# Optimization experiments

Measured on AMD Instinct MI355X. Metric: run time of the kernel, lower is better.

## Reference

```python
import jax, jax.numpy as jnp
import numpy as np

NUM_ROIS = 148
BSZ = 16
HID = 64
IN_CH = 128
OUT_CH = 2
N1, E1 = 131072, 2097152
N2, E2 = 2368, 37888
LRELU_SLOPE = 0.01
BN_EPS = 1e-5


def gcn_conv(x, src, dst, ew, W, b, n):
    """PyG GCNConv with edge weights and self-loops (weight 1): D^-1/2 (A+I) D^-1/2 X W + b."""
    h = x @ W  # (n, out)
    deg = jax.ops.segment_sum(ew, dst, num_segments=n) + 1.0  # self-loop weight 1
    dinv = jax.lax.rsqrt(deg)
    norm = dinv[src] * ew * dinv[dst]  # (E,)
    out = jax.ops.segment_sum(h[src] * norm[:, None], dst, num_segments=n)
    out = out + h * (dinv * dinv)[:, None]  # self-loop term: 1/deg
    return out + b


def roi_pool_mean(x, roi, batch, num_rois, bsz):
    """Segment mean keyed by (batch, roi); empty groups stay zero. Returns (bsz, num_rois*d)."""
    seg = batch * num_rois + roi
    nseg = bsz * num_rois
    sums = jax.ops.segment_sum(x, seg, num_segments=nseg)
    cnt = jax.ops.segment_sum(jnp.ones((x.shape[0],), x.dtype), seg, num_segments=nseg)
    pooled = sums / jnp.maximum(cnt, 1.0)[:, None]
    return pooled.reshape(bsz, -1)


def _params(key):
    ks = jax.random.split(key, 8)
    def lin(k, fi, fo):
        return jax.random.normal(k, (fi, fo), jnp.float32) / np.sqrt(fi)
    p = {}
    p["W1a"], p["b1a"] = lin(ks[0], IN_CH, HID), jnp.zeros((HID,), jnp.float32)
    p["W1b"], p["b1b"] = lin(ks[1], HID, HID), jnp.zeros((HID,), jnp.float32)
    p["W2a"], p["b2a"] = lin(ks[2], IN_CH, HID), jnp.zeros((HID,), jnp.float32)
    p["W2b"], p["b2b"] = lin(ks[3], HID, HID), jnp.zeros((HID,), jnp.float32)
    p["Wm1"], p["bm1"] = lin(ks[4], HID * NUM_ROIS, 1000), jnp.zeros((1000,), jnp.float32)
    p["gamma"], p["beta"] = jnp.ones((1000,), jnp.float32), jnp.zeros((1000,), jnp.float32)
    p["bn_mean"], p["bn_var"] = jnp.zeros((1000,), jnp.float32), jnp.ones((1000,), jnp.float32)
    p["Wm2"], p["bm2"] = lin(ks[5], 1000, OUT_CH), jnp.zeros((OUT_CH,), jnp.float32)
    return p


def setup_inputs() -> dict:
    key = jax.random.key(0)
    ks = jax.random.split(key, 12)
    inp = {
        "x1": jax.random.normal(ks[0], (N1, IN_CH), jnp.float32),
        "node_label": jax.random.randint(ks[1], (N1,), 0, NUM_ROIS, jnp.int32),
        "edge_index1": jax.random.randint(ks[2], (2, E1), 0, N1, jnp.int32),
        "edge_weight1": jax.random.uniform(ks[3], (E1,), jnp.float32),
        "batch1": jnp.sort(jax.random.randint(ks[4], (N1,), 0, BSZ, jnp.int32)),
        "x2": jax.random.normal(ks[5], (N2, IN_CH), jnp.float32),
        "roi_label": jax.random.randint(ks[6], (N2,), 0, NUM_ROIS, jnp.int32),
        "edge_index2": jax.random.randint(ks[7], (2, E2), 0, N2, jnp.int32),
        "edge_weight2": jax.random.uniform(ks[8], (E2,), jnp.float32),
        "batch2": jnp.sort(jax.random.randint(ks[9], (N2,), 0, BSZ, jnp.int32)),
    }
    inp.update(_params(ks[10]))
    return inp


def reference(x1, node_label, edge_index1, edge_weight1, batch1,
              x2, roi_label, edge_index2, edge_weight2, batch2,
              W1a, b1a, W1b, b1b, W2a, b2a, W2b, b2b,
              Wm1, bm1, gamma, beta, bn_mean, bn_var, Wm2, bm2):
    # ROI-graph branch (convs_roi[:-1], eval mode: dropout is identity)
    s2, d2 = edge_index2[0], edge_index2[1]
    h2 = jax.nn.relu(gcn_conv(x2, s2, d2, edge_weight2, W2a, b2a, N2))
    h2 = jax.nn.relu(gcn_conv(h2, s2, d2, edge_weight2, W2b, b2b, N2))
    embedding_roi = roi_pool_mean(h2, roi_label, batch2, NUM_ROIS, BSZ)  # (B, 148*HID)
    # fine-grained branch (convs[:-1])
    s1, d1 = edge_index1[0], edge_index1[1]
    h1 = jax.nn.relu(gcn_conv(x1, s1, d1, edge_weight1, W1a, b1a, N1))
    h1 = jax.nn.relu(gcn_conv(h1, s1, d1, edge_weight1, W1b, b1b, N1))
    embedding = roi_pool_mean(h1, node_label, batch1, NUM_ROIS, BSZ)
    # classifier on embedding + embedding_roi
    s = embedding + embedding_roi
    h = s @ Wm1 + bm1
    h = gamma * (h - bn_mean) * jax.lax.rsqrt(bn_var + BN_EPS) + beta  # BatchNorm1d (eval)
    h = jnp.where(h > 0, h, LRELU_SLOPE * h)  # LeakyReLU
    out = h @ Wm2 + bm2  # (B, OUT_CH)
    return out, embedding, embedding_roi, embedding + embedding_roi
```

## Files before the change

### kernel.cpp

```cpp
#include <hip/hip_runtime.h>
#include <hip/hip_fp16.h>

#define N1 131072
#define E1 2097152
#define N2 2368
#define E2 37888
#define NROIS 148
#define BSZ 16
#define HID 64
#define INCH 128
#define NSEG (BSZ*NROIS)
#define SDIM (NROIS*HID)
#define CLS 1000
#define OCH 2

#define KT1 74
#define KCC 128
#define CT1 4

#define NB1 512
#define BLK1 512
#define EPB (E1/BLK1)
#define NPB (N1/NB1)

#define CB1 ((N1+3)/4)
#define CB2 ((N2+3)/4)
#define PB  ((NSEG+3)/4)

#define T1 (N1/16)
#define T2 (N2/16)
#define GEMMB ((T1+T2)/4)

typedef _Float16 h8 __attribute__((ext_vector_type(8)));
typedef float f4 __attribute__((ext_vector_type(4)));

__device__ __forceinline__ unsigned packh2(float a, float b) {
    return (unsigned)__half_as_ushort(__float2half_rn(a)) |
           ((unsigned)__half_as_ushort(__float2half_rn(b)) << 16);
}

__device__ __forceinline__ void fma_lo(float& a, unsigned hb, float w) {
    asm("v_fma_mix_f32 %0, %1, %2, %0 op_sel:[0,0,0] op_sel_hi:[1,0,0]"
        : "+v"(a) : "v"(hb), "v"(w));
}
__device__ __forceinline__ void fma_hi(float& a, unsigned hb, float w) {
    asm("v_fma_mix_f32 %0, %1, %2, %0 op_sel:[1,0,0] op_sel_hi:[1,0,0]"
        : "+v"(a) : "v"(hb), "v"(w));
}


__global__ void k_hist_dst(int* __restrict__ cnt, const int* __restrict__ dst, int E) {
    int e = blockIdx.x * 256 + threadIdx.x;
    if (e < E) atomicAdd(&cnt[dst[e]], 1);
}

__global__ void k_hist_seg2(int* __restrict__ c1, const int* __restrict__ b1,
                            const int* __restrict__ l1, int n1_,
                            int* __restrict__ c2, const int* __restrict__ b2,
                            const int* __restrict__ l2, int n2_) {
    int i = blockIdx.x * 256 + threadIdx.x;
    if (i < n1_) { atomicAdd(&c1[b1[i] * NROIS + l1[i]], 1); return; }
    int j = i - n1_;
    if (j < n2_) atomicAdd(&c2[b2[j] * NROIS + l2[j]], 1);
}

__global__ void k_scan1(const int* __restrict__ in, int* __restrict__ out,
                        int* __restrict__ part, int n) {
    __shared__ int sh[256];
    int t = threadIdx.x;
    int i0 = blockIdx.x * 1024 + t * 4;
    int v0 = (i0     < n) ? in[i0]     : 0;
    int v1 = (i0 + 1 < n) ? in[i0 + 1] : 0;
    int v2 = (i0 + 2 < n) ? in[i0 + 2] : 0;
    int v3 = (i0 + 3 < n) ? in[i0 + 3] : 0;
    int tot = v0 + v1 + v2 + v3;
    sh[t] = tot; __syncthreads();
    for (int off = 1; off < 256; off <<= 1) {
        int x = 0; if (t >= off) x = sh[t - off];
        __syncthreads();
        if (t >= off) sh[t] += x;
        __syncthreads();
    }
    int excl = sh[t] - tot;
    if (t == 255) part[blockIdx.x] = sh[255];
    if (i0     < n) out[i0]     = excl;
    if (i0 + 1 < n) out[i0 + 1] = excl + v0;
    if (i0 + 2 < n) out[i0 + 2] = excl + v0 + v1;
    if (i0 + 3 < n) out[i0 + 3] = excl + v0 + v1 + v2;
}

__global__ void k_scan2(int* __restrict__ part, int cnt) {
    __shared__ int sh[256];
    int t = threadIdx.x;
    int v = (t < cnt) ? part[t] : 0;
    sh[t] = v; __syncthreads();
    for (int off = 1; off < 256; off <<= 1) {
        int x = 0; if (t >= off) x = sh[t - off];
        __syncthreads();
        if (t >= off) sh[t] += x;
        __syncthreads();
    }
    if (t < cnt) part[t] = sh[t] - v;
}

__global__ void k_scan3(int* __restrict__ out, const int* __restrict__ part, int n, int total) {
    int i = blockIdx.x * 256 + threadIdx.x;
    if (i < n) out[i] += part[i >> 10];
    if (i == 0) out[n] = total;
}

__global__ void k_scan_one(const int* __restrict__ in0, int* __restrict__ out0,
                           int* __restrict__ oo0, int n0,
                           const int* __restrict__ in1, int* __restrict__ out1,
                           int* __restrict__ oo1, int n1_) {
    __shared__ int sh[256];
    __shared__ int carry;
    const int* in; int* out; int* oo; int n;
    if (blockIdx.x == 0) { in = in0; out = out0; oo = oo0; n = n0; }
    else { if (!in1) return; in = in1; out = out1; oo = oo1; n = n1_; }
    int t = threadIdx.x;
    if (t == 0) carry = 0;
    __syncthreads();
    for (int base = 0; base < n; base += 256) {
        int i = base + t;
        int v = (i < n) ? in[i] : 0;
        sh[t] = v; __syncthreads();
        for (int off = 1; off < 256; off <<= 1) {
            int x = 0; if (t >= off) x = sh[t - off];
            __syncthreads();
            if (t >= off) sh[t] += x;
            __syncthreads();
        }
        if (i < n) {
            int e = carry + sh[t] - v;
            out[i] = e;
            if (oo) oo[i] = e;
        }
        __syncthreads();
        if (t == 255) carry += sh[255];
        __syncthreads();
    }
    if (t == 0) out[n] = carry;
}

__global__ void k_fill_edges(int2* __restrict__ edges, int* __restrict__ off,
                             const int* __restrict__ src, const int* __restrict__ dst,
                             const float* __restrict__ ew, int E) {
    int e = blockIdx.x * 256 + threadIdx.x;
    if (e >= E) return;
    int pos = atomicAdd(&off[dst[e]], 1);
    edges[pos] = make_int2(src[e], __float_as_int(ew[e]));
}

__global__ void k_fill_seg2(int* __restrict__ id1, int* __restrict__ o1,
                            const int* __restrict__ b1, const int* __restrict__ l1, int n1_,
                            int* __restrict__ id2, int* __restrict__ o2,
                            const int* __restrict__ b2, const int* __restrict__ l2, int n2_) {
    int i = blockIdx.x * 256 + threadIdx.x;
    if (i < n1_) {
        int pos = atomicAdd(&o1[b1[i] * NROIS + l1[i]], 1);
        id1[pos] = i << 7;
        return;
    }
    int j = i - n1_;
    if (j < n2_) {
        int pos = atomicAdd(&o2[b2[j] * NROIS + l2[j]], 1);
        id2[pos] = j << 7;
    }
}

__global__ void k_deg_dinv(float* __restrict__ dinv, const int* __restrict__ row,
                           const int2* __restrict__ edges, int n) {
    int d = blockIdx.x * 256 + threadIdx.x;
    if (d >= n) return;
    int a = row[d], b = row[d + 1];
    float s = 1.0f;
    for (int i = a; i < b; i++) s += __int_as_float(edges[i].y);
    dinv[d] = rsqrtf(s);
}

__global__ void k_scale(int2* __restrict__ edges, const int* __restrict__ row,
                        const float* __restrict__ dinv, int n) {
    int d = blockIdx.x * 256 + threadIdx.x;
    if (d >= n) return;
    int a = row[d], b = row[d + 1];
    float dd = dinv[d];
    for (int i = a; i < b; i++) {
        int2 e = edges[i];
        edges[i] = make_int2(e.x << 7,
                             __float_as_int(dinv[e.x] * __int_as_float(e.y) * dd));
    }
}


__global__ __launch_bounds__(256) void k_p1(int* __restrict__ bh, const int* __restrict__ dst) {
    __shared__ int cnt[NB1];
    int t = threadIdx.x, blk = blockIdx.x;
    for (int i = t; i < NB1; i += 256) cnt[i] = 0;
    __syncthreads();
    int base = blk * EPB;
    for (int i = t; i < EPB; i += 256) atomicAdd(&cnt[dst[base + i] >> 8], 1);
    __syncthreads();
    for (int b = t; b < NB1; b += 256) bh[b * BLK1 + blk] = cnt[b];
}

__global__ __launch_bounds__(256) void k_p2(int2* __restrict__ tmp, const int* __restrict__ obh,
                                            const int* __restrict__ src,
                                            const int* __restrict__ dst,
                                            const float* __restrict__ ew) {
    __shared__ int cur[NB1];
    int t = threadIdx.x, blk = blockIdx.x;
    for (int b = t; b < NB1; b += 256) cur[b] = obh[b * BLK1 + blk];
    __syncthreads();
    int base = blk * EPB;
    for (int i = t; i < EPB; i += 256) {
        int e = base + i;
        int d = dst[e];
        int pos = atomicAdd(&cur[d >> 8], 1);
        tmp[pos] = make_int2(src[e] | ((d & 255) << 17), __float_as_int(ew[e]));
    }
}

__global__ __launch_bounds__(256) void k_p3a(int* __restrict__ row1, float* __restrict__ dinv,
                                             const int2* __restrict__ tmp,
                                             const int* __restrict__ obh) {
    __shared__ int h[NPB];
    __shared__ float ws[NPB];
    __shared__ int sc[256];
    int t = threadIdx.x, b = blockIdx.x;
    h[t] = 0; ws[t] = 0.f;
    __syncthreads();
    int ebase = obh[b * BLK1];
    int eend  = (b == NB1 - 1) ? E1 : obh[(b + 1) * BLK1];
    for (int i = ebase + t; i < eend; i += 256) {
        int2 ed = tmp[i];
        int dl = (ed.x >> 17) & 255;
        atomicAdd(&h[dl], 1);
        atomicAdd(&ws[dl], __int_as_float(ed.y));
    }
    __syncthreads();
    int cnt = h[t];
    sc[t] = cnt; __syncthreads();
    for (int off = 1; off < 256; off <<= 1) {
        int x = 0; if (t >= off) x = sc[t - off];
        __syncthreads();
        if (t >= off) sc[t] += x;
        __syncthreads();
    }
    row1[b * NPB + t] = ebase + sc[t] - cnt;
    dinv[b * NPB + t] = rsqrtf(1.f + ws[t]);
    if (b == NB1 - 1 && t == 255) row1[N1] = E1;
}

__global__ __launch_bounds__(256) void k_p3b(int2* __restrict__ edges,
                                             const int2* __restrict__ tmp,
                                             const int* __restrict__ obh,
                                             const int* __restrict__ row,
                                             const float* __restrict__ dinv) {
    __shared__ int cur[NPB];
    __shared__ float dvl[NPB];
    int t = threadIdx.x, b = blockIdx.x;
    int n0 = b * NPB;
    for (int i = t; i < NPB; i += 256) {
        cur[i] = row[n0 + i];
        dvl[i] = dinv[n0 + i];
    }
    __syncthreads();
    int a  = obh[b * BLK1];
    int e_ = (b == NB1 - 1) ? E1 : obh[(b + 1) * BLK1];
    for (int i = a + t; i < e_; i += 256) {
        int2 ed = tmp[i];
        int dl = (ed.x >> 17) & 255;
        int s = ed.x & 0x1FFFF;
        int pos = atomicAdd(&cur[dl], 1);
        float w = dinv[s] * __int_as_float(ed.y) * dvl[dl];
        edges[pos] = make_int2(s << 7, __float_as_int(w));
    }
}


__device__ __forceinline__ void wfrag(uint4* __restrict__ o, const float* __restrict__ W,
                                      int KCH, int idx) {
    int lane = idx & 63;
    int rest = idx >> 6;
    int ch = rest % KCH;
    int ct = rest / KCH;
    int kr = ch * 32 + ((lane >> 4) * 8);
    int col = ct * 16 + (lane & 15);
    const float* wp = W + (size_t)kr * 64 + col;
    o[idx] = make_uint4(packh2(wp[0],   wp[64]),
                        packh2(wp[128], wp[192]),
                        packh2(wp[256], wp[320]),
                        packh2(wp[384], wp[448]));
}

__global__ void k_wprep(uint4* __restrict__ wf1a, const float* __restrict__ W1a,
                        uint4* __restrict__ wf1b, const float* __restrict__ W1b,
                        uint4* __restrict__ wf2a, const float* __restrict__ W2a,
                        uint4* __restrict__ wf2b, const float* __restrict__ W2b) {
    int idx = blockIdx.x * 256 + threadIdx.x;
    if      (idx < 1024) wfrag(wf1a, W1a, 4, idx);
    else if (idx < 1536) wfrag(wf1b, W1b, 2, idx - 1024);
    else if (idx < 2560) wfrag(wf2a, W2a, 4, idx - 1536);
    else if (idx < 3072) wfrag(wf2b, W2b, 2, idx - 2560);
}

__device__ __forceinline__ h8 loadA(const float* p) {
    float4 a = *(const float4*)p;
    float4 b = *(const float4*)(p + 4);
    union { h8 v; __half h[8]; } u;
    u.h[0] = __float2half_rn(a.x); u.h[1] = __float2half_rn(a.y);
    u.h[2] = __float2half_rn(a.z); u.h[3] = __float2half_rn(a.w);
    u.h[4] = __float2half_rn(b.x); u.h[5] = __float2half_rn(b.y);
    u.h[6] = __float2half_rn(b.z); u.h[7] = __float2half_rn(b.w);
    return u.v;
}
__device__ __forceinline__ h8 loadA(const __half* p) {
    union { h8 v; uint4 u; } u;
    u.u = *(const uint4*)p;
    return u.v;
}

template <int K, typename T>
__global__ __launch_bounds__(256) void k_gemm(__half* __restrict__ out1, const T* __restrict__ x1,
                                              const uint4* __restrict__ wfa, int t1,
                                              __half* __restrict__ out2, const T* __restrict__ x2,
                                              const uint4* __restrict__ wfb, int t2) {
    constexpr int KCH = K / 32;
    int wid = blockIdx.x * 4 + (threadIdx.x >> 6);
    int lane = threadIdx.x & 63;
    __half* out; const T* x; const uint4* wf; int row0;
    if (wid < t1) { out = out1; x = x1; wf = wfa; row0 = wid * 16; }
    else {
        int w2 = wid - t1;
        if (w2 >= t2) return;
        out = out2; x = x2; wf = wfb; row0 = w2 * 16;
    }
    int lrow = lane & 15, lg = lane >> 4;

    h8 bf[4][KCH];
#pragma unroll
    for (int ct = 0; ct < 4; ct++)
#pragma unroll
        for (int ch = 0; ch < KCH; ch++) {
            union { h8 v; uint4 u; } u;
            u.u = wf[(ct * KCH + ch) * 64 + lane];
            bf[ct][ch] = u.v;
        }

    const T* xr = x + (size_t)(row0 + lrow) * K + lg * 8;
    h8 af[KCH];
#pragma unroll
    for (int ch = 0; ch < KCH; ch++) af[ch] = loadA(xr + ch * 32);

    f4 acc[4];
#pragma unroll
    for (int ct = 0; ct < 4; ct++) acc[ct] = (f4){0.f, 0.f, 0.f, 0.f};
#pragma unroll
    for (int ch = 0; ch < KCH; ch++)
#pragma unroll
        for (int ct = 0; ct < 4; ct++)
            acc[ct] = __builtin_amdgcn_mfma_f32_16x16x32_f16(af[ch], bf[ct][ch], acc[ct], 0, 0, 0);

#pragma unroll
    for (int ct = 0; ct < 4; ct++)
#pragma unroll
        for (int r = 0; r < 4; r++)
            out[(size_t)(row0 + lg * 4 + r) * 64 + ct * 16 + lrow] = __float2half_rn(acc[ct][r]);
}


__device__ __forceinline__ void conv_core(__half* __restrict__ out, const __half* __restrict__ h,
                                          const int2* __restrict__ edges,
                                          const int* __restrict__ row,
                                          const float* __restrict__ dinv,
                                          const float* __restrict__ bias, int d, int lane) {
    int slot = lane >> 4;
    int f4i = lane & 15;
    const char* hb = (const char*)(h + f4i * 4);
    int a = row[d], b = row[d + 1];
    float acc0[4] = {0.f, 0.f, 0.f, 0.f};
    float acc1[4] = {0.f, 0.f, 0.f, 0.f};

    int base = a;
    for (; base + 64 <= b; base += 64) {
        int2 e = edges[base + lane];
        int sv = e.x, wv = e.y;
#pragma unroll
        for (int j = 0; j < 64; j += 8) {
            int   s0 = __shfl(sv, j + slot);
            float w0 = __int_as_float(__shfl(wv, j + slot));
            int   s1 = __shfl(sv, j + 4 + slot);
            float w1 = __int_as_float(__shfl(wv, j + 4 + slot));
            uint2 h0 = *(const uint2*)(hb + (unsigned)s0);
            uint2 h1 = *(const uint2*)(hb + (unsigned)s1);
            fma_lo(acc0[0], h0.x, w0); fma_hi(acc0[1], h0.x, w0);
            fma_lo(acc0[2], h0.y, w0); fma_hi(acc0[3], h0.y, w0);
            fma_lo(acc1[0], h1.x, w1); fma_hi(acc1[1], h1.x, w1);
            fma_lo(acc1[2], h1.y, w1); fma_hi(acc1[3], h1.y, w1);
        }
    }
    if (base < b) {
        int m = b - base;
        int sv = 0, wv = 0;
        if (base + lane < b) { int2 e = edges[base + lane]; sv = e.x; wv = e.y; }
        for (int j = 0; j < m; j += 8) {
            int   s0 = __shfl(sv, j + slot);
            float w0 = __int_as_float(__shfl(wv, j + slot));
            int   s1 = __shfl(sv, j + 4 + slot);
            float w1 = __int_as_float(__shfl(wv, j + 4 + slot));
            uint2 h0 = *(const uint2*)(hb + (unsigned)s0);
            uint2 h1 = *(const uint2*)(hb + (unsigned)s1);
            fma_lo(acc0[0], h0.x, w0); fma_hi(acc0[1], h0.x, w0);
            fma_lo(acc0[2], h0.y, w0); fma_hi(acc0[3], h0.y, w0);
            fma_lo(acc1[0], h1.x, w1); fma_hi(acc1[1], h1.x, w1);
            fma_lo(acc1[2], h1.y, w1); fma_hi(acc1[3], h1.y, w1);
        }
    }
    float r0 = acc0[0] + acc1[0];
    float r1 = acc0[1] + acc1[1];
    float r2 = acc0[2] + acc1[2];
    float r3 = acc0[3] + acc1[3];
    r0 += __shfl_xor(r0, 16); r0 += __shfl_xor(r0, 32);
    r1 += __shfl_xor(r1, 16); r1 += __shfl_xor(r1, 32);
    r2 += __shfl_xor(r2, 16); r2 += __shfl_xor(r2, 32);
    r3 += __shfl_xor(r3, 16); r3 += __shfl_xor(r3, 32);
    if (slot == 0) {
        float di = dinv[d];
        float sl = di * di;
        uint2 hd = *(const uint2*)(hb + ((unsigned)d << 7));
        fma_lo(r0, hd.x, sl); fma_hi(r1, hd.x, sl);
        fma_lo(r2, hd.y, sl); fma_hi(r3, hd.y, sl);
        float4 bb = *(const float4*)(bias + f4i * 4);
        r0 = fmaxf(r0 + bb.x, 0.f);
        r1 = fmaxf(r1 + bb.y, 0.f);
        r2 = fmaxf(r2 + bb.z, 0.f);
        r3 = fmaxf(r3 + bb.w, 0.f);
        uint2 ov;
        ov.x = packh2(r0, r1);
        ov.y = packh2(r2, r3);
        *(uint2*)(out + (size_t)d * HID + f4i * 4) = ov;
    }
}

__global__ __launch_bounds__(256) void k_conv(__half* __restrict__ o1, const __half* __restrict__ h1,
                                              const int2* __restrict__ e1, const int* __restrict__ r1,
                                              const float* __restrict__ dv1, const float* __restrict__ bi1,
                                              int n1_, int nb1_,
                                              __half* __restrict__ o2, const __half* __restrict__ h2,
                                              const int2* __restrict__ e2, const int* __restrict__ r2,
                                              const float* __restrict__ dv2, const float* __restrict__ bi2,
                                              int n2_) {
    int blk = blockIdx.x;
    int lane = threadIdx.x & 63;
    int w = threadIdx.x >> 6;
    if (blk < nb1_) {
        int d = blk * 4 + w;
        if (d < n1_) conv_core(o1, h1, e1, r1, dv1, bi1, d, lane);
    } else {
        int d = (blk - nb1_) * 4 + w;
        if (d < n2_) conv_core(o2, h2, e2, r2, dv2, bi2, d, lane);
    }
}

__device__ __forceinline__ void pool_core(float* __restrict__ emb, const __half* __restrict__ h,
                                          const int* __restrict__ nodeid,
                                          const int* __restrict__ segrow, int s, int lane) {
    int slot = lane >> 4;
    int f4i = lane & 15;
    const char* hb = (const char*)(h + f4i * 4);
    int a = segrow[s], b = segrow[s + 1];
    float acc[4][4];
#pragma unroll
    for (int k = 0; k < 4; k++)
#pragma unroll
        for (int f = 0; f < 4; f++) acc[k][f] = 0.f;

    int i = a;
    for (; i + 16 <= b; i += 16) {
#pragma unroll
        for (int k = 0; k < 4; k++) {
            int q = nodeid[i + 4 * k + slot];
            uint2 hv = *(const uint2*)(hb + (unsigned)q);
            fma_lo(acc[k][0], hv.x, 1.f); fma_hi(acc[k][1], hv.x, 1.f);
            fma_lo(acc[k][2], hv.y, 1.f); fma_hi(acc[k][3], hv.y, 1.f);
        }
    }
    if (i < b) {
#pragma unroll
        for (int k = 0; k < 4; k++) {
            int idx = i + 4 * k + slot;
            int q = nodeid[min(idx, b - 1)];
            float w = (idx < b) ? 1.f : 0.f;
            uint2 hv = *(const uint2*)(hb + (unsigned)q);
            fma_lo(acc[k][0], hv.x, w); fma_hi(acc[k][1], hv.x, w);
            fma_lo(acc[k][2], hv.y, w); fma_hi(acc[k][3], hv.y, w);
        }
    }
    float r0 = (acc[0][0] + acc[1][0]) + (acc[2][0] + acc[3][0]);
    float r1 = (acc[0][1] + acc[1][1]) + (acc[2][1] + acc[3][1]);
    float r2 = (acc[0][2] + acc[1][2]) + (acc[2][2] + acc[3][2]);
    float r3 = (acc[0][3] + acc[1][3]) + (acc[2][3] + acc[3][3]);
    r0 += __shfl_xor(r0, 16); r0 += __shfl_xor(r0, 32);
    r1 += __shfl_xor(r1, 16); r1 += __shfl_xor(r1, 32);
    r2 += __shfl_xor(r2, 16); r2 += __shfl_xor(r2, 32);
    r3 += __shfl_xor(r3, 16); r3 += __shfl_xor(r3, 32);
    if (slot == 0) {
        float inv = 1.0f / fmaxf((float)(b - a), 1.0f);
        float4 mv = make_float4(r0 * inv, r1 * inv, r2 * inv, r3 * inv);
        *(float4*)(emb + (size_t)s * HID + f4i * 4) = mv;
    }
}

__global__ __launch_bounds__(256) void k_pool(float* __restrict__ em1, const __half* __restrict__ h1,
                                              const int* __restrict__ id1, const int* __restrict__ sr1,
                                              int nbs,
                                              float* __restrict__ em2, const __half* __restrict__ h2,
                                              const int* __restrict__ id2, const int* __restrict__ sr2) {
    int blk = blockIdx.x;
    int lane = threadIdx.x & 63;
    int w = threadIdx.x >> 6;
    if (blk < nbs) {
        int s = blk * 4 + w;
        if (s < NSEG) pool_core(em1, h1, id1, sr1, s, lane);
    } else {
        int s = (blk - nbs) * 4 + w;
        if (s < NSEG) pool_core(em2, h2, id2, sr2, s, lane);
    }
}


__global__ __launch_bounds__(256) void k_cls(float* __restrict__ part_,
                                             const float* __restrict__ e1,
                                             const float* __restrict__ e2,
                                             float* __restrict__ esum,
                                             const float* __restrict__ Wm1) {
    __shared__ float sl[KCC * 16];
    int tid = threadIdx.x;
    int kt = blockIdx.x >> 2, ct = blockIdx.x & 3;
    int k0 = kt * KCC;
    bool wr = (ct == 0);
    for (int i = tid; i < KCC * 16; i += 256) {
        int kk = i & (KCC - 1), b = i >> 7;
        int idx = b * SDIM + k0 + kk;
        float v = e1[idx] + e2[idx];
        sl[kk * 16 + b] = v;
        if (wr) esum[idx] = v;
    }
    __syncthreads();
    int c = ct * 256 + tid;
    bool active = c < CLS;
    float acc[16];
#pragma unroll
    for (int b = 0; b < 16; b++) acc[b] = 0.f;
    const float* wp = Wm1 + (size_t)k0 * CLS + c;
#pragma unroll 2
    for (int kk = 0; kk < KCC; kk++) {
        float w = active ? wp[(size_t)kk * CLS] : 0.f;
        float4 s0 = *(const float4*)(&sl[kk * 16 + 0]);
        float4 s1 = *(const float4*)(&sl[kk * 16 + 4]);
        float4 s2 = *(const float4*)(&sl[kk * 16 + 8]);
        float4 s3 = *(const float4*)(&sl[kk * 16 + 12]);
        acc[0]  += s0.x * w; acc[1]  += s0.y * w; acc[2]  += s0.z * w; acc[3]  += s0.w * w;
        acc[4]  += s1.x * w; acc[5]  += s1.y * w; acc[6]  += s1.z * w; acc[7]  += s1.w * w;
        acc[8]  += s2.x * w; acc[9]  += s2.y * w; acc[10] += s2.z * w; acc[11] += s2.w * w;
        acc[12] += s3.x * w; acc[13] += s3.y * w; acc[14] += s3.z * w; acc[15] += s3.w * w;
    }
    float* pp = part_ + (size_t)(kt * CT1 + ct) * 16 * 256;
#pragma unroll
    for (int b = 0; b < 16; b++) pp[b * 256 + tid] = acc[b];
}

__global__ void k_credbn(float* __restrict__ hact, const float* __restrict__ part_,
                         const float* __restrict__ bm1, const float* __restrict__ gamma,
                         const float* __restrict__ beta, const float* __restrict__ mean,
                         const float* __restrict__ var) {
    int idx = blockIdx.x * 256 + threadIdx.x;
    if (idx >= BSZ * CLS) return;
    int b = idx / CLS, c = idx % CLS;
    int ct = c >> 8, cl = c & 255;
    float sum = 0.f;
#pragma unroll 2
    for (int kt = 0; kt < KT1; kt++)
        sum += part_[((size_t)(kt * CT1 + ct) * 16 + b) * 256 + cl];
    float t = sum + bm1[c];
    t = gamma[c] * (t - mean[c]) * rsqrtf(var[c] + 1e-5f) + beta[c];
    hact[idx] = t > 0.f ? t : 0.01f * t;
}

__global__ void k_out(float* __restrict__ outp, const float* __restrict__ hact,
                      const float* __restrict__ Wm2, const float* __restrict__ bm2) {
    int b = blockIdx.x;
    int tid = threadIdx.x;
    int o = tid & 1, part = tid >> 1;
    float acc = (part == 0) ? bm2[o] : 0.f;
    for (int k = part; k < CLS; k += 128) acc += hact[b * CLS + k] * Wm2[k * OCH + o];
    unsafeAtomicAdd(&outp[b * OCH + o], acc);
}

extern "C" void kernel_launch(void* const* d_in, const int* in_sizes, int n_in,
                              void* d_out, int out_size, void* d_ws, size_t ws_size,
                              hipStream_t stream) {
    const float* x1  = (const float*)d_in[0];
    const int*   nl  = (const int*)d_in[1];
    const int*   ei1 = (const int*)d_in[2];
    const float* ew1 = (const float*)d_in[3];
    const int*   ba1 = (const int*)d_in[4];
    const float* x2  = (const float*)d_in[5];
    const int*   rl  = (const int*)d_in[6];
    const int*   ei2 = (const int*)d_in[7];
    const float* ew2 = (const float*)d_in[8];
    const int*   ba2 = (const int*)d_in[9];
    const float* W1a = (const float*)d_in[10];
    const float* b1a = (const float*)d_in[11];
    const float* W1b = (const float*)d_in[12];
    const float* b1b = (const float*)d_in[13];
    const float* W2a = (const float*)d_in[14];
    const float* b2a = (const float*)d_in[15];
    const float* W2b = (const float*)d_in[16];
    const float* b2b = (const float*)d_in[17];
    const float* Wm1 = (const float*)d_in[18];
    const float* bm1 = (const float*)d_in[19];
    const float* gam = (const float*)d_in[20];
    const float* bet = (const float*)d_in[21];
    const float* bmn = (const float*)d_in[22];
    const float* bvr = (const float*)d_in[23];
    const float* Wm2 = (const float*)d_in[24];
    const float* bm2 = (const float*)d_in[25];

    float* out  = (float*)d_out;
    float* emb1 = out + 32;
    float* emb2 = emb1 + NSEG * HID;
    float* esum = emb2 + NSEG * HID;

    char* p = (char*)d_ws;
    auto carve = [&](size_t nbytes) { char* q = p; p += (nbytes + 255) & ~(size_t)255; return (void*)q; };
    int*    row1    = (int*)   carve((N1 + 1) * 4);
    int2*   edges1  = (int2*)  carve((size_t)E1 * 8);
    float*  dinv1   = (float*) carve(N1 * 4);
    __half* A1h     = (__half*)carve((size_t)N1 * HID * 2);
    __half* B1h     = (__half*)carve((size_t)N1 * HID * 2);
    int*    nodeid1 = (int*)   carve(N1 * 4);
    int*    segrow1 = (int*)   carve((NSEG + 1) * 4);
    int*    segoff  = (int*)   carve(2 * NSEG * 4);
    int*    bh      = (int*)   carve((NB1 * BLK1 + 1) * 4);
    int*    obh     = (int*)   carve((NB1 * BLK1 + 1) * 4);
    int*    row2    = (int*)   carve((N2 + 1) * 4);
    int*    off2    = (int*)   carve(N2 * 4);
    int2*   edges2  = (int2*)  carve((size_t)E2 * 8);
    float*  dinv2   = (float*) carve(N2 * 4);
    __half* A2h     = (__half*)carve((size_t)N2 * HID * 2);
    __half* B2h     = (__half*)carve((size_t)N2 * HID * 2);
    int*    nodeid2 = (int*)   carve(N2 * 4);
    int*    segrow2 = (int*)   carve((NSEG + 1) * 4);
    int*    part    = (int*)   carve(256 * 4);
    float*  hact    = (float*) carve(BSZ * CLS * 4);
    uint4*  wf1a    = (uint4*) carve(1024 * 16);
    uint4*  wf1b    = (uint4*) carve(512 * 16);
    uint4*  wf2a    = (uint4*) carve(1024 * 16);
    uint4*  wf2b    = (uint4*) carve(512 * 16);
    int*    segoff1 = segoff;
    int*    segoff2 = segoff + NSEG;
    int2*  tmp1 = (int2*)B1h;
    float* clsp = (float*)B1h;

    const int* src1 = ei1;
    const int* dst1 = ei1 + E1;
    const int* src2 = ei2;
    const int* dst2 = ei2 + E2;

    hipMemsetAsync(d_out, 0, (size_t)out_size * sizeof(float), stream);

    k_wprep<<<12, 256, 0, stream>>>(wf1a, W1a, wf1b, W1b, wf2a, W2a, wf2b, W2b);

    hipMemsetAsync(off2, 0, N2 * 4, stream);
    k_hist_dst<<<(E2 + 255) / 256, 256, 0, stream>>>(off2, dst2, E2);
    k_scan_one<<<1, 256, 0, stream>>>(off2, row2, off2, N2, nullptr, nullptr, nullptr, 0);
    k_fill_edges<<<(E2 + 255) / 256, 256, 0, stream>>>(edges2, off2, src2, dst2, ew2, E2);
    k_deg_dinv<<<(N2 + 255) / 256, 256, 0, stream>>>(dinv2, row2, edges2, N2);
    k_scale<<<(N2 + 255) / 256, 256, 0, stream>>>(edges2, row2, dinv2, N2);

    k_p1<<<BLK1, 256, 0, stream>>>(bh, dst1);
    k_scan1<<<(NB1 * BLK1 + 1023) / 1024, 256, 0, stream>>>(bh, obh, part, NB1 * BLK1);
    k_scan2<<<1, 256, 0, stream>>>(part, (NB1 * BLK1 + 1023) / 1024);
    k_scan3<<<(NB1 * BLK1 + 255) / 256, 256, 0, stream>>>(obh, part, NB1 * BLK1, E1);
    k_p2<<<BLK1, 256, 0, stream>>>(tmp1, obh, src1, dst1, ew1);
    k_p3a<<<NB1, 256, 0, stream>>>(row1, dinv1, tmp1, obh);
    k_p3b<<<NB1, 256, 0, stream>>>(edges1, tmp1, obh, row1, dinv1);

    k_gemm<INCH, float><<<GEMMB, 256, 0, stream>>>(A1h, x1, wf1a, T1, A2h, x2, wf2a, T2);
    k_conv<<<CB1 + CB2, 256, 0, stream>>>(B1h, A1h, edges1, row1, dinv1, b1a, N1, CB1,
                                          B2h, A2h, edges2, row2, dinv2, b2a, N2);
    k_gemm<HID, __half><<<GEMMB, 256, 0, stream>>>(A1h, B1h, wf1b, T1, A2h, B2h, wf2b, T2);
    k_conv<<<CB1 + CB2, 256, 0, stream>>>(B1h, A1h, edges1, row1, dinv1, b1b, N1, CB1,
                                          B2h, A2h, edges2, row2, dinv2, b2b, N2);

    hipMemsetAsync(segoff, 0, 2 * NSEG * 4, stream);
    k_hist_seg2<<<(N1 + N2 + 255) / 256, 256, 0, stream>>>(segoff1, ba1, nl, N1,
                                                           segoff2, ba2, rl, N2);
    k_scan_one<<<2, 256, 0, stream>>>(segoff1, segrow1, segoff1, NSEG,
                                      segoff2, segrow2, segoff2, NSEG);
    k_fill_seg2<<<(N1 + N2 + 255) / 256, 256, 0, stream>>>(nodeid1, segoff1, ba1, nl, N1,
                                                           nodeid2, segoff2, ba2, rl, N2);
    k_pool<<<PB + PB, 256, 0, stream>>>(emb1, B1h, nodeid1, segrow1, PB,
                                        emb2, B2h, nodeid2, segrow2);

    k_cls<<<KT1 * CT1, 256, 0, stream>>>(clsp, emb1, emb2, esum, Wm1);
    k_credbn<<<(BSZ * CLS + 255) / 256, 256, 0, stream>>>(hact, clsp, bm1, gam, bet, bmn, bvr);
    k_out<<<BSZ, 256, 0, stream>>>(out, hact, Wm2, bm2);
}
```

Baseline: 564.6 us.

## Map four destination nodes per wavefront with 16-byte feature gathers in conv and pool

The conv and pool kernels now give each wavefront four destinations (or segments) instead of one. Each 16-lane group handles one node: two edge halves of eight lanes each, with every lane loading eight fp16 features as a uint4. This targets the low-degree graph (about 16 edges per node on average), where a full 64-lane wave per node left most lanes idle and needed a long shuffle reduction. The cost is a data-dependent inner loop per group, which can diverge when degrees differ inside a wave, and the pool kernel on long segments loses the wider per-wave parallelism it had before.

```diff
diff --git a/kernel.cpp b/kernel.cpp
--- a/kernel.cpp
+++ b/kernel.cpp
@@ -23,9 +23,9 @@
 #define EPB (E1/BLK1)
 #define NPB (N1/NB1)
 
-#define CB1 ((N1+3)/4)
-#define CB2 ((N2+3)/4)
-#define PB  ((NSEG+3)/4)
+#define CW1 ((N1+15)/16)
+#define CW2 ((N2+15)/16)
+#define PW  ((NSEG+15)/16)
 
 #define T1 (N1/16)
 #define T2 (N2/16)
@@ -369,77 +369,58 @@
             out[(size_t)(row0 + lg * 4 + r) * 64 + ct * 16 + lrow] = __float2half_rn(acc[ct][r]);
 }
 
-
-__device__ __forceinline__ void conv_core(__half* __restrict__ out, const __half* __restrict__ h,
+__device__ __forceinline__ void conv_wave(__half* __restrict__ out, const __half* __restrict__ h,
                                           const int2* __restrict__ edges,
                                           const int* __restrict__ row,
                                           const float* __restrict__ dinv,
-                                          const float* __restrict__ bias, int d, int lane) {
-    int slot = lane >> 4;
-    int f4i = lane & 15;
-    const char* hb = (const char*)(h + f4i * 4);
-    int a = row[d], b = row[d + 1];
-    float acc0[4] = {0.f, 0.f, 0.f, 0.f};
-    float acc1[4] = {0.f, 0.f, 0.f, 0.f};
-
-    int base = a;
-    for (; base + 64 <= b; base += 64) {
-        int2 e = edges[base + lane];
-        int sv = e.x, wv = e.y;
-#pragma unroll
-        for (int j = 0; j < 64; j += 8) {
-            int   s0 = __shfl(sv, j + slot);
-            float w0 = __int_as_float(__shfl(wv, j + slot));
-            int   s1 = __shfl(sv, j + 4 + slot);
-            float w1 = __int_as_float(__shfl(wv, j + 4 + slot));
-            uint2 h0 = *(const uint2*)(hb + (unsigned)s0);
-            uint2 h1 = *(const uint2*)(hb + (unsigned)s1);
-            fma_lo(acc0[0], h0.x, w0); fma_hi(acc0[1], h0.x, w0);
-            fma_lo(acc0[2], h0.y, w0); fma_hi(acc0[3], h0.y, w0);
-            fma_lo(acc1[0], h1.x, w1); fma_hi(acc1[1], h1.x, w1);
-            fma_lo(acc1[2], h1.y, w1); fma_hi(acc1[3], h1.y, w1);
+                                          const float* __restrict__ bias,
+                                          int d0, int n, int lane) {
+    int g  = lane >> 4;
+    int fl = lane & 15;
+    int eh = fl >> 3;
+    int f8 = fl & 7;
+    int d  = d0 + g;
+    bool vn = d < n;
+    int a = 0, b = 0;
+    if (vn) { a = row[d]; b = row[d + 1]; }
+    const char* hb = (const char*)h + f8 * 16;
+    float acc[8] = {0.f,0.f,0.f,0.f,0.f,0.f,0.f,0.f};
+
+    for (int base = a; base < b; base += 16) {
+        int sv = 0, wv = 0;
+        if (base + fl < b) { int2 e = edges[base + fl]; sv = e.x; wv = e.y; }
+        int mm = b - base; if (mm > 16) mm = 16;
+        int steps = (mm + 1) >> 1;
+        int idx = (g << 4) + eh;
+        for (int t = 0; t < steps; t++) {
+            int   s = __shfl(sv, idx + (t << 1));
+            float w = __int_as_float(__shfl(wv, idx + (t << 1)));
+            uint4 hv = *(const uint4*)(hb + (unsigned)s);
+            fma_lo(acc[0], hv.x, w); fma_hi(acc[1], hv.x, w);
+            fma_lo(acc[2], hv.y, w); fma_hi(acc[3], hv.y, w);
+            fma_lo(acc[4], hv.z, w); fma_hi(acc[5], hv.z, w);
+            fma_lo(acc[6], hv.w, w); fma_hi(acc[7], hv.w, w);
         }
     }
-    if (base < b) {
-        int m = b - base;
-        int sv = 0, wv = 0;
-        if (base + lane < b) { int2 e = edges[base + lane]; sv = e.x; wv = e.y; }
-        for (int j = 0; j < m; j += 8) {
-            int   s0 = __shfl(sv, j + slot);
-            float w0 = __int_as_float(__shfl(wv, j + slot));
-            int   s1 = __shfl(sv, j + 4 + slot);
-            float w1 = __int_as_float(__shfl(wv, j + 4 + slot));
-            uint2 h0 = *(const uint2*)(hb + (unsigned)s0);
-            uint2 h1 = *(const uint2*)(hb + (unsigned)s1);
-            fma_lo(acc0[0], h0.x, w0); fma_hi(acc0[1], h0.x, w0);
-            fma_lo(acc0[2], h0.y, w0); fma_hi(acc0[3], h0.y, w0);
-            fma_lo(acc1[0], h1.x, w1); fma_hi(acc1[1], h1.x, w1);
-            fma_lo(acc1[2], h1.y, w1); fma_hi(acc1[3], h1.y, w1);
-        }
-    }
-    float r0 = acc0[0] + acc1[0];
-    float r1 = acc0[1] + acc1[1];
-    float r2 = acc0[2] + acc1[2];
-    float r3 = acc0[3] + acc1[3];
-    r0 += __shfl_xor(r0, 16); r0 += __shfl_xor(r0, 32);
-    r1 += __shfl_xor(r1, 16); r1 += __shfl_xor(r1, 32);
-    r2 += __shfl_xor(r2, 16); r2 += __shfl_xor(r2, 32);
-    r3 += __shfl_xor(r3, 16); r3 += __shfl_xor(r3, 32);
-    if (slot == 0) {
+    float r[8];
+#pragma unroll
+    for (int f = 0; f < 8; f++) r[f] = acc[f] + __shfl_xor(acc[f], 8);
+    if (vn && eh == 0) {
         float di = dinv[d];
         float sl = di * di;
-        uint2 hd = *(const uint2*)(hb + ((unsigned)d << 7));
-        fma_lo(r0, hd.x, sl); fma_hi(r1, hd.x, sl);
-        fma_lo(r2, hd.y, sl); fma_hi(r3, hd.y, sl);
-        float4 bb = *(const float4*)(bias + f4i * 4);
-        r0 = fmaxf(r0 + bb.x, 0.f);
-        r1 = fmaxf(r1 + bb.y, 0.f);
-        r2 = fmaxf(r2 + bb.z, 0.f);
-        r3 = fmaxf(r3 + bb.w, 0.f);
-        uint2 ov;
-        ov.x = packh2(r0, r1);
-        ov.y = packh2(r2, r3);
-        *(uint2*)(out + (size_t)d * HID + f4i * 4) = ov;
+        uint4 hd = *(const uint4*)(hb + ((unsigned)d << 7));
+        fma_lo(r[0], hd.x, sl); fma_hi(r[1], hd.x, sl);
+        fma_lo(r[2], hd.y, sl); fma_hi(r[3], hd.y, sl);
+        fma_lo(r[4], hd.z, sl); fma_hi(r[5], hd.z, sl);
+        fma_lo(r[6], hd.w, sl); fma_hi(r[7], hd.w, sl);
+        float4 b0 = *(const float4*)(bias + f8 * 8);
+        float4 b1 = *(const float4*)(bias + f8 * 8 + 4);
+        uint4 ov;
+        ov.x = packh2(fmaxf(r[0] + b0.x, 0.f), fmaxf(r[1] + b0.y, 0.f));
+        ov.y = packh2(fmaxf(r[2] + b0.z, 0.f), fmaxf(r[3] + b0.w, 0.f));
+        ov.z = packh2(fmaxf(r[4] + b1.x, 0.f), fmaxf(r[5] + b1.y, 0.f));
+        ov.w = packh2(fmaxf(r[6] + b1.z, 0.f), fmaxf(r[7] + b1.w, 0.f));
+        *(uint4*)(out + (size_t)d * HID + f8 * 8) = ov;
     }
 }
 
@@ -453,62 +434,50 @@
                                               int n2_) {
     int blk = blockIdx.x;
     int lane = threadIdx.x & 63;
-    int w = threadIdx.x >> 6;
-    if (blk < nb1_) {
-        int d = blk * 4 + w;
-        if (d < n1_) conv_core(o1, h1, e1, r1, dv1, bi1, d, lane);
-    } else {
-        int d = (blk - nb1_) * 4 + w;
-        if (d < n2_) conv_core(o2, h2, e2, r2, dv2, bi2, d, lane);
-    }
-}
-
-__device__ __forceinline__ void pool_core(float* __restrict__ emb, const __half* __restrict__ h,
+    int wv = threadIdx.x >> 6;
+    if (blk < nb1_) conv_wave(o1, h1, e1, r1, dv1, bi1, blk * 16 + wv * 4, n1_, lane);
+    else            conv_wave(o2, h2, e2, r2, dv2, bi2, (blk - nb1_) * 16 + wv * 4, n2_, lane);
+}
+
+__device__ __forceinline__ void pool_wave(float* __restrict__ emb, const __half* __restrict__ h,
                                           const int* __restrict__ nodeid,
-                                          const int* __restrict__ segrow, int s, int lane) {
-    int slot = lane >> 4;
-    int f4i = lane & 15;
-    const char* hb = (const char*)(h + f4i * 4);
-    int a = segrow[s], b = segrow[s + 1];
-    float acc[4][4];
-#pragma unroll
-    for (int k = 0; k < 4; k++)
-#pragma unroll
-        for (int f = 0; f < 4; f++) acc[k][f] = 0.f;
-
-    int i = a;
-    for (; i + 16 <= b; i += 16) {
-#pragma unroll
-        for (int k = 0; k < 4; k++) {
-            int q = nodeid[i + 4 * k + slot];
-            uint2 hv = *(const uint2*)(hb + (unsigned)q);
-            fma_lo(acc[k][0], hv.x, 1.f); fma_hi(acc[k][1], hv.x, 1.f);
-            fma_lo(acc[k][2], hv.y, 1.f); fma_hi(acc[k][3], hv.y, 1.f);
+                                          const int* __restrict__ segrow, int s0, int lane) {
+    int g  = lane >> 4;
+    int fl = lane & 15;
+    int eh = fl >> 3;
+    int f8 = fl & 7;
+    int s  = s0 + g;
+    bool vs = s < NSEG;
+    int a = 0, b = 0;
+    if (vs) { a = segrow[s]; b = segrow[s + 1]; }
+    const char* hb = (const char*)h + f8 * 16;
+    float acc[8] = {0.f,0.f,0.f,0.f,0.f,0.f,0.f,0.f};
+
+    for (int base = a; base < b; base += 16) {
+        int sv = 0, wv = 0;
+        if (base + fl < b) { sv = nodeid[base + fl]; wv = 0x3f800000; }
+        int mm = b - base; if (mm > 16) mm = 16;
+        int steps = (mm + 1) >> 1;
+        int idx = (g << 4) + eh;
+        for (int t = 0; t < steps; t++) {
+            int   q = __shfl(sv, idx + (t << 1));
+            float w = __int_as_float(__shfl(wv, idx + (t << 1)));
+            uint4 hv = *(const uint4*)(hb + (unsigned)q);
+            fma_lo(acc[0], hv.x, w); fma_hi(acc[1], hv.x, w);
+            fma_lo(acc[2], hv.y, w); fma_hi(acc[3], hv.y, w);
+            fma_lo(acc[4], hv.z, w); fma_hi(acc[5], hv.z, w);
+            fma_lo(acc[6], hv.w, w); fma_hi(acc[7], hv.w, w);
         }
     }
-    if (i < b) {
-#pragma unroll
-        for (int k = 0; k < 4; k++) {
-            int idx = i + 4 * k + slot;
-            int q = nodeid[min(idx, b - 1)];
-            float w = (idx < b) ? 1.f : 0.f;
-            uint2 hv = *(const uint2*)(hb + (unsigned)q);
-            fma_lo(acc[k][0], hv.x, w); fma_hi(acc[k][1], hv.x, w);
-            fma_lo(acc[k][2], hv.y, w); fma_hi(acc[k][3], hv.y, w);
-        }
-    }
-    float r0 = (acc[0][0] + acc[1][0]) + (acc[2][0] + acc[3][0]);
-    float r1 = (acc[0][1] + acc[1][1]) + (acc[2][1] + acc[3][1]);
-    float r2 = (acc[0][2] + acc[1][2]) + (acc[2][2] + acc[3][2]);
-    float r3 = (acc[0][3] + acc[1][3]) + (acc[2][3] + acc[3][3]);
-    r0 += __shfl_xor(r0, 16); r0 += __shfl_xor(r0, 32);
-    r1 += __shfl_xor(r1, 16); r1 += __shfl_xor(r1, 32);
-    r2 += __shfl_xor(r2, 16); r2 += __shfl_xor(r2, 32);
-    r3 += __shfl_xor(r3, 16); r3 += __shfl_xor(r3, 32);
-    if (slot == 0) {
+    float r[8];
+#pragma unroll
+    for (int f = 0; f < 8; f++) r[f] = acc[f] + __shfl_xor(acc[f], 8);
+    if (vs && eh == 0) {
         float inv = 1.0f / fmaxf((float)(b - a), 1.0f);
-        float4 mv = make_float4(r0 * inv, r1 * inv, r2 * inv, r3 * inv);
-        *(float4*)(emb + (size_t)s * HID + f4i * 4) = mv;
+        float4 lo = make_float4(r[0] * inv, r[1] * inv, r[2] * inv, r[3] * inv);
+        float4 hi = make_float4(r[4] * inv, r[5] * inv, r[6] * inv, r[7] * inv);
+        *(float4*)(emb + (size_t)s * HID + f8 * 8)     = lo;
+        *(float4*)(emb + (size_t)s * HID + f8 * 8 + 4) = hi;
     }
 }
 
@@ -519,14 +488,9 @@
                                               const int* __restrict__ id2, const int* __restrict__ sr2) {
     int blk = blockIdx.x;
     int lane = threadIdx.x & 63;
-    int w = threadIdx.x >> 6;
-    if (blk < nbs) {
-        int s = blk * 4 + w;
-        if (s < NSEG) pool_core(em1, h1, id1, sr1, s, lane);
-    } else {
-        int s = (blk - nbs) * 4 + w;
-        if (s < NSEG) pool_core(em2, h2, id2, sr2, s, lane);
-    }
+    int wv = threadIdx.x >> 6;
+    if (blk < nbs) pool_wave(em1, h1, id1, sr1, blk * 16 + wv * 4, lane);
+    else           pool_wave(em2, h2, id2, sr2, (blk - nbs) * 16 + wv * 4, lane);
 }
 
 
@@ -689,10 +653,10 @@
     k_p3b<<<NB1, 256, 0, stream>>>(edges1, tmp1, obh, row1, dinv1);
 
     k_gemm<INCH, float><<<GEMMB, 256, 0, stream>>>(A1h, x1, wf1a, T1, A2h, x2, wf2a, T2);
-    k_conv<<<CB1 + CB2, 256, 0, stream>>>(B1h, A1h, edges1, row1, dinv1, b1a, N1, CB1,
+    k_conv<<<CW1 + CW2, 256, 0, stream>>>(B1h, A1h, edges1, row1, dinv1, b1a, N1, CW1,
                                           B2h, A2h, edges2, row2, dinv2, b2a, N2);
     k_gemm<HID, __half><<<GEMMB, 256, 0, stream>>>(A1h, B1h, wf1b, T1, A2h, B2h, wf2b, T2);
-    k_conv<<<CB1 + CB2, 256, 0, stream>>>(B1h, A1h, edges1, row1, dinv1, b1b, N1, CB1,
+    k_conv<<<CW1 + CW2, 256, 0, stream>>>(B1h, A1h, edges1, row1, dinv1, b1b, N1, CW1,
                                           B2h, A2h, edges2, row2, dinv2, b2b, N2);
 
     hipMemsetAsync(segoff, 0, 2 * NSEG * 4, stream);
@@ -702,7 +666,7 @@
                                       segoff2, segrow2, segoff2, NSEG);
     k_fill_seg2<<<(N1 + N2 + 255) / 256, 256, 0, stream>>>(nodeid1, segoff1, ba1, nl, N1,
                                                            nodeid2, segoff2, ba2, rl, N2);
-    k_pool<<<PB + PB, 256, 0, stream>>>(emb1, B1h, nodeid1, segrow1, PB,
+    k_pool<<<PW + PW, 256, 0, stream>>>(emb1, B1h, nodeid1, segrow1, PW,
                                         emb2, B2h, nodeid2, segrow2);
 
     k_cls<<<KT1 * CT1, 256, 0, stream>>>(clsp, emb1, emb2, esum, Wm1);
```

Measured after the change: 556.4 us. Within noise of the previous version (-1.5%).
